# Performance work log

Hardware: AMD Instinct MI355X
Metric: run time of the kernel (lower is better)

Reference implementation:

```python
import jax, jax.numpy as jnp
import numpy as np

N_NODES = 500000
N_GRAPHS = 10000
D_FEAT = 256


def setup_inputs() -> dict:
    key = jax.random.key(0)
    k1, k2, k3, k4, k5 = jax.random.split(key, 5)
    states = jax.random.normal(k1, (N_NODES, D_FEAT), dtype=jnp.float32)
    # ragged row lengths summing exactly to N_NODES
    rng = np.random.default_rng(0)
    sizes = rng.multinomial(N_NODES, np.ones(N_GRAPHS) / N_GRAPHS).astype(np.int32)
    graph_sizes = jnp.asarray(sizes)
    # Dense(1) gate and Dense(2) output layer params (glorot-ish init)
    gate_w = jax.random.normal(k2, (D_FEAT, 1), dtype=jnp.float32) / np.sqrt(D_FEAT)
    gate_b = jnp.zeros((1,), dtype=jnp.float32)
    out_w = jax.random.normal(k3, (D_FEAT, 2), dtype=jnp.float32) / np.sqrt(D_FEAT)
    out_b = jnp.zeros((2,), dtype=jnp.float32)
    return {"states": states, "graph_sizes": graph_sizes,
            "gate_w": gate_w, "gate_b": gate_b,
            "out_w": out_w, "out_b": out_b}


def reference(states, graph_sizes, gate_w, gate_b, out_w, out_b):
    n_graphs = graph_sizes.shape[0]
    n_nodes = states.shape[0]
    # segment id for each node, derived from ragged row lengths
    seg_ids = jnp.repeat(jnp.arange(n_graphs, dtype=jnp.int32), graph_sizes,
                         total_repeat_length=n_nodes)
    # gate logits: Dense(1) then squeeze -> [N]
    gate = (states @ gate_w + gate_b)[:, 0]
    # faithful ragged_softmax: subtract GLOBAL max (as in the TF code), exp,
    # normalize per segment with +1e-16
    gate = jnp.exp(gate - jnp.max(gate))
    seg_sums = jax.ops.segment_sum(gate, seg_ids, num_segments=n_graphs)  # [G]
    gate = gate / (seg_sums[seg_ids] + 1e-16)
    # Dense(2) outputs weighted by gate, summed per graph -> [G, 2]
    outputs = (states @ out_w + out_b) * gate[:, None]
    return jax.ops.segment_sum(outputs, seg_ids, num_segments=n_graphs)
```

## Files before the change

kernel.cpp:

```cpp
#include <hip/hip_runtime.h>
#include <hip/hip_bf16.h>

#define D_FEAT_K 256

typedef float floatx4 __attribute__((ext_vector_type(4)));

__global__ void scan_kernel(const int* __restrict__ sizes,
                            int* __restrict__ offsets,
                            int n) {
    __shared__ int wsum[16];
    __shared__ int chunk_carry;
    const int tid  = threadIdx.x;
    const int lane = tid & 63;
    const int wid  = tid >> 6;
    if (tid == 0) chunk_carry = 0;
    __syncthreads();
    for (int base = 0; base < n; base += 1024) {
        const int i = base + tid;
        const int v = (i < n) ? sizes[i] : 0;
        int s = v;
#pragma unroll
        for (int d = 1; d < 64; d <<= 1) {
            int t = __shfl_up(s, d);
            if (lane >= d) s += t;
        }
        if (lane == 63) wsum[wid] = s;
        __syncthreads();
        if (wid == 0 && lane < 16) {
            int w = wsum[lane];
#pragma unroll
            for (int d = 1; d < 16; d <<= 1) {
                int t = __shfl_up(w, d);
                if (lane >= d) w += t;
            }
            wsum[lane] = w;
        }
        __syncthreads();
        const int waveoff = (wid == 0) ? 0 : wsum[wid - 1];
        if (i < n) offsets[i] = chunk_carry + waveoff + s - v;
        const int total = wsum[15];
        __syncthreads();
        if (tid == 0) chunk_carry += total;
        __syncthreads();
    }
}

__global__ __launch_bounds__(256)
void fused_kernel(const float* __restrict__ states,
                  const float* __restrict__ gate_w,
                  const float* __restrict__ gate_b,
                  const float* __restrict__ out_w,
                  const float* __restrict__ out_b,
                  const int* __restrict__ offsets,
                  const int* __restrict__ sizes,
                  float2* __restrict__ outp,
                  int n_graphs) {
    const int wid  = threadIdx.x >> 6;
    const int lane = threadIdx.x & 63;
    const int g = blockIdx.x * 4 + wid;
    if (g >= n_graphs) return;

    const int q   = lane & 15;
    const int grp = lane >> 4;

    float4 gw[4], owA[4], owB[4];
#pragma unroll
    for (int k = 0; k < 4; ++k) {
        const int f0 = 4 * q + 64 * k;
        gw[k]  = *reinterpret_cast<const float4*>(gate_w + f0);
        owA[k] = *reinterpret_cast<const float4*>(out_w + 2 * f0);
        owB[k] = *reinterpret_cast<const float4*>(out_w + 2 * f0 + 4);
    }
    const float gb  = gate_b[0];
    const int   off = offsets[g];
    const int   sz  = sizes[g];

    float se = 0.f, s0 = 0.f, s1 = 0.f;
    for (int r = grp; r < sz; r += 4) {
        const float* row = states + (size_t)(off + r) * D_FEAT_K;
        float pl = 0.f, p0 = 0.f, p1 = 0.f;
#pragma unroll
        for (int k = 0; k < 4; ++k) {
            floatx4 s = __builtin_nontemporal_load(
                reinterpret_cast<const floatx4*>(row + 4 * q + 64 * k));
            pl += s.x * gw[k].x  + s.y * gw[k].y  + s.z * gw[k].z  + s.w * gw[k].w;
            p0 += s.x * owA[k].x + s.y * owA[k].z + s.z * owB[k].x + s.w * owB[k].z;
            p1 += s.x * owA[k].y + s.y * owA[k].w + s.z * owB[k].y + s.w * owB[k].w;
        }
#pragma unroll
        for (int m = 8; m >= 1; m >>= 1) pl += __shfl_xor(pl, m);
        const float e = expf(pl + gb);
        se += e;
        s0 += p0 * e;
        s1 += p1 * e;
    }
#pragma unroll
    for (int m = 32; m >= 1; m >>= 1) {
        se += __shfl_xor(se, m);
        s0 += __shfl_xor(s0, m);
        s1 += __shfl_xor(s1, m);
    }
    if (lane == 0) {
        const float S   = se * 0.0625f;
        const float inv = 1.0f / (S + 1e-16f);
        outp[g] = make_float2((s0 + out_b[0] * S) * inv,
                              (s1 + out_b[1] * S) * inv);
    }
}

extern "C" void kernel_launch(void* const* d_in, const int* in_sizes, int n_in,
                              void* d_out, int out_size, void* d_ws, size_t ws_size,
                              hipStream_t stream) {
    const float* states      = (const float*)d_in[0];
    const int*   graph_sizes = (const int*)d_in[1];
    const float* gate_w      = (const float*)d_in[2];
    const float* gate_b      = (const float*)d_in[3];
    const float* out_w       = (const float*)d_in[4];
    const float* out_b       = (const float*)d_in[5];

    const int n_graphs = in_sizes[1];

    int* offsets = (int*)d_ws;

    scan_kernel<<<1, 1024, 0, stream>>>(graph_sizes, offsets, n_graphs);

    fused_kernel<<<(n_graphs + 3) / 4, 256, 0, stream>>>(
        states, gate_w, gate_b, out_w, out_b,
        offsets, graph_sizes, (float2*)d_out, n_graphs);
}
```

Baseline: 92.83 us.

## Drop separate scan kernel; compute segment offsets per wave via redundant prefix sum

```diff
diff --git a/kernel.cpp b/kernel.cpp
--- a/kernel.cpp
+++ b/kernel.cpp
@@ -5,60 +5,34 @@
 
 typedef float floatx4 __attribute__((ext_vector_type(4)));
 
-__global__ void scan_kernel(const int* __restrict__ sizes,
-                            int* __restrict__ offsets,
-                            int n) {
-    __shared__ int wsum[16];
-    __shared__ int chunk_carry;
-    const int tid  = threadIdx.x;
-    const int lane = tid & 63;
-    const int wid  = tid >> 6;
-    if (tid == 0) chunk_carry = 0;
-    __syncthreads();
-    for (int base = 0; base < n; base += 1024) {
-        const int i = base + tid;
-        const int v = (i < n) ? sizes[i] : 0;
-        int s = v;
-#pragma unroll
-        for (int d = 1; d < 64; d <<= 1) {
-            int t = __shfl_up(s, d);
-            if (lane >= d) s += t;
-        }
-        if (lane == 63) wsum[wid] = s;
-        __syncthreads();
-        if (wid == 0 && lane < 16) {
-            int w = wsum[lane];
-#pragma unroll
-            for (int d = 1; d < 16; d <<= 1) {
-                int t = __shfl_up(w, d);
-                if (lane >= d) w += t;
-            }
-            wsum[lane] = w;
-        }
-        __syncthreads();
-        const int waveoff = (wid == 0) ? 0 : wsum[wid - 1];
-        if (i < n) offsets[i] = chunk_carry + waveoff + s - v;
-        const int total = wsum[15];
-        __syncthreads();
-        if (tid == 0) chunk_carry += total;
-        __syncthreads();
-    }
-}
-
 __global__ __launch_bounds__(256)
 void fused_kernel(const float* __restrict__ states,
+                  const int* __restrict__ sizes,
                   const float* __restrict__ gate_w,
                   const float* __restrict__ gate_b,
                   const float* __restrict__ out_w,
                   const float* __restrict__ out_b,
-                  const int* __restrict__ offsets,
-                  const int* __restrict__ sizes,
                   float2* __restrict__ outp,
                   int n_graphs) {
     const int wid  = threadIdx.x >> 6;
     const int lane = threadIdx.x & 63;
     const int g = blockIdx.x * 4 + wid;
     if (g >= n_graphs) return;
+
+    int acc = 0;
+    {
+        const int nv = g >> 2;
+        const int4* s4 = reinterpret_cast<const int4*>(sizes);
+        for (int j = lane; j < nv; j += 64) {
+            int4 v = s4[j];
+            acc += v.x + v.y + v.z + v.w;
+        }
+        for (int j = (nv << 2) + lane; j < g; j += 64) acc += sizes[j];
+#pragma unroll
+        for (int m = 32; m >= 1; m >>= 1) acc += __shfl_xor(acc, m);
+    }
+    const int off = acc;
+    const int sz  = sizes[g];
 
     const int q   = lane & 15;
     const int grp = lane >> 4;
@@ -71,9 +45,7 @@
         owA[k] = *reinterpret_cast<const float4*>(out_w + 2 * f0);
         owB[k] = *reinterpret_cast<const float4*>(out_w + 2 * f0 + 4);
     }
-    const float gb  = gate_b[0];
-    const int   off = offsets[g];
-    const int   sz  = sizes[g];
+    const float gb = gate_b[0];
 
     float se = 0.f, s0 = 0.f, s1 = 0.f;
     for (int r = grp; r < sz; r += 4) {
@@ -89,7 +61,7 @@
         }
 #pragma unroll
         for (int m = 8; m >= 1; m >>= 1) pl += __shfl_xor(pl, m);
-        const float e = expf(pl + gb);
+        const float e = __expf(pl + gb);
         se += e;
         s0 += p0 * e;
         s1 += p1 * e;
@@ -120,11 +92,7 @@
 
     const int n_graphs = in_sizes[1];
 
-    int* offsets = (int*)d_ws;
-
-    scan_kernel<<<1, 1024, 0, stream>>>(graph_sizes, offsets, n_graphs);
-
     fused_kernel<<<(n_graphs + 3) / 4, 256, 0, stream>>>(
-        states, gate_w, gate_b, out_w, out_b,
-        offsets, graph_sizes, (float2*)d_out, n_graphs);
+        states, graph_sizes, gate_w, gate_b, out_w, out_b,
+        (float2*)d_out, n_graphs);
 }
```

Result: faster. 89.25 us (-3.9%).
